# Kernel optimization log

Hardware: AMD Instinct MI355X
Metric: run time of the kernel (lower is better)

The kernel has to match this reference:

```python
import jax, jax.numpy as jnp
import numpy as np

NUM_HEADS = 8
HEAD_DIM = 64
D_MODEL = NUM_HEADS * HEAD_DIM  # 512
B, T = 4, 2048


def setup_inputs() -> dict:
    key = jax.random.key(0)
    k1, k2 = jax.random.split(key)
    x = jax.random.normal(k1, (B, T, D_MODEL), dtype=jnp.float32)
    mask = jnp.ones((B, 1, T, T), dtype=jnp.float32)
    W = jax.random.normal(k2, (D_MODEL, 3 * D_MODEL), dtype=jnp.float32) * (D_MODEL ** -0.5)
    b = jnp.zeros((3 * D_MODEL,), dtype=jnp.float32)
    return {"x": x, "mask": mask, "W": W, "b": b}


def reference(x, mask, W, b):
    batch = x.shape[0]
    # fused QKV projection: [B, T, 3D]
    qkv = jnp.einsum("btd,de->bte", x, W) + b
    # NOTE: faithful to torch reshape [B, T, H, Hd, 3] -> the size-3 axis is innermost
    qkv = qkv.reshape(batch, -1, NUM_HEADS, HEAD_DIM, 3)
    qkv = jnp.transpose(qkv, (4, 0, 2, 1, 3))  # [3, B, H, T, Hd]
    q, k, v = qkv[0], qkv[1], qkv[2]
    logits = jnp.einsum("bhqd,bhkd->bhqk", q, k) / (HEAD_DIM ** 0.5)
    logits = logits + (1.0 - mask) * -10000.0
    w = jax.nn.softmax(logits, axis=-1)
    out = jnp.einsum("bhqk,bhkd->bhqd", w, v)  # [B, H, T, Hd]
    out = jnp.transpose(out, (0, 2, 1, 3)).reshape(batch, -1, NUM_HEADS * HEAD_DIM)
    return out
```

## Files before the change

kernel.cpp:

```cpp
#include <hip/hip_runtime.h>
#include <hip/hip_bf16.h>
#include <stdint.h>

#define B_   4
#define T_   2048
#define H_   8
#define HD_  64
#define DM_  512
#define N3_  1536

typedef short bf_el;
typedef __attribute__((ext_vector_type(8))) bf_el bfrag;
typedef __attribute__((ext_vector_type(4))) float ffrag;

#define SCALE_L2E  0.18033688011112043f
#define MASK_L2E   14426.950408889634f

static __device__ __forceinline__ unsigned short f2bf(float f) {
    union { float f; unsigned int i; } v; v.f = f;
    unsigned int r = v.i + 0x7fff + ((v.i >> 16) & 1);
    return (unsigned short)(r >> 16);
}
static __device__ __forceinline__ unsigned short f2bf_fast(float f) {
    union { float f; unsigned int i; } v; v.f = f;
    return (unsigned short)((v.i + 0x8000u) >> 16);
}

__global__ __launch_bounds__(256) void k_prep(const float* __restrict__ W,
                                              const float* __restrict__ X,
                                              const float* __restrict__ mask,
                                              unsigned short* __restrict__ Wt,
                                              unsigned short* __restrict__ Xb,
                                              int* __restrict__ flags) {
    __shared__ __align__(16) unsigned short Ls[64 * 72];
    const int bid = blockIdx.x;
    const int tid = threadIdx.x;

    if (bid < 512) {
        const int wave = tid >> 6, lane = tid & 63;
        const int e  = bid >> 2;
        const int g  = bid & 3;
        const int mb = e >> 5, qt = e & 31;
#pragma unroll
        for (int w2 = 0; w2 < 2; ++w2) {
            const int kt = g * 8 + wave * 2 + w2;
            unsigned int acc = 0u;
#pragma unroll
            for (int j = 0; j < 16; ++j) {
                const int row = j * 4 + (lane >> 4);
                const uint4 u = *(const uint4*)(mask + ((size_t)mb * T_ + qt * 64 + row) * T_
                                                     + kt * 64 + (lane & 15) * 4);
                acc |= (u.x ^ 0x3F800000u) | (u.y ^ 0x3F800000u) |
                       (u.z ^ 0x3F800000u) | (u.w ^ 0x3F800000u);
            }
            unsigned long long bal = __ballot(acc != 0u);
            if (lane == 0) flags[e * 32 + kt] = (bal != 0ULL) ? 1 : 0;
        }
        return;
    }
    if (bid < 768) {
        const int b2 = bid - 512;
        const float* src = X + (size_t)b2 * 16384;
        unsigned short* dst = Xb + (size_t)b2 * 16384;
#pragma unroll
        for (int j = 0; j < 8; ++j) {
            int idx = j * 512 + tid * 2;
            float4 f0 = *(const float4*)(src + idx * 4);
            float4 f1 = *(const float4*)(src + idx * 4 + 4);
            __align__(16) unsigned short t8[8];
            t8[0] = f2bf_fast(f0.x); t8[1] = f2bf_fast(f0.y);
            t8[2] = f2bf_fast(f0.z); t8[3] = f2bf_fast(f0.w);
            t8[4] = f2bf_fast(f1.x); t8[5] = f2bf_fast(f1.y);
            t8[6] = f2bf_fast(f1.z); t8[7] = f2bf_fast(f1.w);
            *(uint4*)(dst + idx * 4) = *(const uint4*)t8;
        }
        return;
    }
    {
        const int t  = bid - 768;
        const int n0 = (t % 24) * 64;
        const int k0 = (t / 24) * 64;
#pragma unroll
        for (int i = 0; i < 4; ++i) {
            int chunk = tid + i * 256;
            int k = chunk >> 4;
            int c = chunk & 15;
            float4 f = *(const float4*)(W + (size_t)(k0 + k) * N3_ + n0 + c * 4);
            unsigned short* p = Ls + k * 72 + c * 4;
            p[0] = f2bf(f.x); p[1] = f2bf(f.y); p[2] = f2bf(f.z); p[3] = f2bf(f.w);
        }
        __syncthreads();
        const int n = tid >> 2;
        const int g = tid & 3;
        __align__(16) unsigned short tmp[16];
#pragma unroll
        for (int i = 0; i < 16; ++i) tmp[i] = Ls[(g * 16 + i) * 72 + n];
        uint4* dst = (uint4*)(Wt + (size_t)(n0 + n) * DM_ + k0 + g * 16);
        dst[0] = *(const uint4*)(tmp);
        dst[1] = *(const uint4*)(tmp + 8);
    }
}

__global__ __launch_bounds__(256) void k_gemm_qkv(const unsigned short* __restrict__ Xb,
                                                  const unsigned short* __restrict__ Wt,
                                                  const float* __restrict__ bias,
                                                  unsigned short* __restrict__ Qb,
                                                  unsigned short* __restrict__ Kb,
                                                  unsigned short* __restrict__ Vtb) {
    __shared__ __align__(16) unsigned short SH[12800];
    unsigned short* As = SH;
    unsigned short* Bs = SH + 5120;
    unsigned short* Cs = SH;

    const int tid  = threadIdx.x;
    const int wave = tid >> 6;
    const int lane = tid & 63;
    const int quad = lane >> 4;
    const int l16  = lane & 15;
    const int wm = wave >> 1, wn = wave & 1;
    const int m0 = blockIdx.y * 128;
    const int h  = blockIdx.x;
    const int n0 = h * 192;

    float bvv[6];
#pragma unroll
    for (int ni = 0; ni < 6; ++ni) bvv[ni] = bias[n0 + wn * 96 + ni * 16 + l16];

    ffrag acc[4][6];
#pragma unroll
    for (int i = 0; i < 4; ++i)
#pragma unroll
        for (int j = 0; j < 6; ++j) acc[i][j] = (ffrag){0.f, 0.f, 0.f, 0.f};

    for (int kt = 0; kt < 16; ++kt) {
        __syncthreads();
#pragma unroll
        for (int i = 0; i < 2; ++i) {
            int chunk = tid + i * 256;
            int r = chunk >> 2, c = chunk & 3;
            *(uint4*)(As + r * 40 + c * 8) =
                *(const uint4*)(Xb + (size_t)(m0 + r) * DM_ + kt * 32 + c * 8);
        }
#pragma unroll
        for (int i = 0; i < 3; ++i) {
            int chunk = tid + i * 256;
            int r = chunk >> 2, c = chunk & 3;
            *(uint4*)(Bs + r * 40 + c * 8) =
                *(const uint4*)(Wt + (size_t)(n0 + r) * DM_ + kt * 32 + c * 8);
        }
        __syncthreads();
        bfrag af[4], bfr[6];
#pragma unroll
        for (int mi = 0; mi < 4; ++mi)
            af[mi] = *(const bfrag*)(As + (wm * 64 + mi * 16 + l16) * 40 + quad * 8);
#pragma unroll
        for (int ni = 0; ni < 6; ++ni)
            bfr[ni] = *(const bfrag*)(Bs + (wn * 96 + ni * 16 + l16) * 40 + quad * 8);
#pragma unroll
        for (int mi = 0; mi < 4; ++mi)
#pragma unroll
            for (int ni = 0; ni < 6; ++ni)
                acc[mi][ni] = __builtin_amdgcn_mfma_f32_16x16x32_bf16(af[mi], bfr[ni], acc[mi][ni], 0, 0, 0);
    }

    const int b   = m0 >> 11;
    const int tb0 = m0 & 2047;
    const size_t bh = (size_t)(b * 8 + h);
    float cscale[6];
#pragma unroll
    for (int ni = 0; ni < 6; ++ni) {
        int c = wn * 96 + ni * 16 + l16;
        cscale[ni] = (c % 3 == 0) ? SCALE_L2E : 1.0f;
    }
#pragma unroll
    for (int half = 0; half < 2; ++half) {
        __syncthreads();
        if (wm == half) {
#pragma unroll
            for (int mi = 0; mi < 4; ++mi)
#pragma unroll
                for (int ni = 0; ni < 6; ++ni)
#pragma unroll
                    for (int reg = 0; reg < 4; ++reg) {
                        int r = mi * 16 + quad * 4 + reg;
                        int c = wn * 96 + ni * 16 + l16;
                        Cs[r * 200 + c] = f2bf_fast((acc[mi][ni][reg] + bvv[ni]) * cscale[ni]);
                    }
        }
        __syncthreads();
        const int tb = tb0 + half * 64;
#pragma unroll
        for (int i = 0; i < 2; ++i) {
            int idx = tid + i * 256;
            int tl = idx >> 3, hc = (idx & 7) * 8;
            __align__(16) unsigned short tq[8], tk[8];
#pragma unroll
            for (int j = 0; j < 8; ++j) {
                tq[j] = Cs[tl * 200 + (hc + j) * 3 + 0];
                tk[j] = Cs[tl * 200 + (hc + j) * 3 + 1];
            }
            *(uint4*)(Qb + (bh * T_ + tb + tl) * HD_ + hc) = *(const uint4*)tq;
            *(uint4*)(Kb + (bh * T_ + tb + tl) * HD_ + hc) = *(const uint4*)tk;
        }
#pragma unroll
        for (int i = 0; i < 2; ++i) {
            int idx = tid + i * 256;
            int hd = idx >> 3, t8 = (idx & 7) * 8;
            __align__(16) unsigned short tv[8];
#pragma unroll
            for (int j = 0; j < 8; ++j)
                tv[j] = Cs[(t8 + j) * 200 + hd * 3 + 2];
            *(uint4*)(Vtb + (bh * HD_ + hd) * T_ + tb + t8) = *(const uint4*)tv;
        }
    }
}

__global__ __launch_bounds__(256) void k_attn(const unsigned short* __restrict__ Q,
                                              const unsigned short* __restrict__ K,
                                              const unsigned short* __restrict__ Vt,
                                              const float* __restrict__ mask,
                                              const int* __restrict__ flags,
                                              float* __restrict__ out) {
    __shared__ __align__(16) unsigned short Ks[64 * 72];
    __shared__ __align__(16) unsigned short Vs[64 * 72];
    __shared__ __align__(16) unsigned short Ps[4][16 * 72];

    const int tid = threadIdx.x;
    const int wave = tid >> 6, lane = tid & 63;
    const int quad = lane >> 4, l16 = lane & 15;
    const int bh = blockIdx.y, b = bh >> 3, h = bh & 7;
    const int qt = blockIdx.x;
    const int q0 = qt * 128;

    bfrag qf[2][2];
#pragma unroll
    for (int g = 0; g < 2; ++g) {
        size_t qrow = ((size_t)bh * T_ + q0 + wave * 32 + g * 16 + l16) * HD_;
        qf[g][0] = *(const bfrag*)(Q + qrow + quad * 8);
        qf[g][1] = *(const bfrag*)(Q + qrow + 32 + quad * 8);
    }
    float lsum[2][4] = {{0.f,0.f,0.f,0.f},{0.f,0.f,0.f,0.f}};
    ffrag of[2][4];
#pragma unroll
    for (int g = 0; g < 2; ++g)
#pragma unroll
        for (int nb = 0; nb < 4; ++nb) of[g][nb] = (ffrag){0.f, 0.f, 0.f, 0.f};

    const int fbase0 = (b * 32 + qt * 2) * 32;
    const int fbase1 = (b * 32 + qt * 2 + 1) * 32;

    for (int kt = 0; kt < 32; ++kt) {
        __syncthreads();
#pragma unroll
        for (int i = 0; i < 2; ++i) {
            int chunk = tid + i * 256;
            int r = chunk >> 3, c = chunk & 7;
            *(uint4*)(Ks + r * 72 + c * 8) =
                *(const uint4*)(K + ((size_t)bh * T_ + kt * 64 + r) * HD_ + c * 8);
            *(uint4*)(Vs + r * 72 + c * 8) =
                *(const uint4*)(Vt + ((size_t)bh * HD_ + r) * T_ + kt * 64 + c * 8);
        }
        int fl[2];
        fl[0] = flags[fbase0 + kt];
        fl[1] = flags[fbase1 + kt];
        __syncthreads();
        bfrag vf[2][4];
#pragma unroll
        for (int ks = 0; ks < 2; ++ks)
#pragma unroll
            for (int nb = 0; nb < 4; ++nb)
                vf[ks][nb] = *(const bfrag*)(Vs + (nb * 16 + l16) * 72 + (ks * 4 + quad) * 8);

#pragma unroll
        for (int g = 0; g < 2; ++g) {
            ffrag sf[4];
#pragma unroll
            for (int ns = 0; ns < 4; ++ns) {
                ffrag a = (ffrag){0.f, 0.f, 0.f, 0.f};
#pragma unroll
                for (int ks = 0; ks < 2; ++ks) {
                    bfrag kf = *(const bfrag*)(Ks + (ns * 16 + l16) * 72 + (ks * 4 + quad) * 8);
                    a = __builtin_amdgcn_mfma_f32_16x16x32_bf16(qf[g][ks], kf, a, 0, 0, 0);
                }
                sf[ns] = a;
            }
            if (fl[g]) {
#pragma unroll
                for (int reg = 0; reg < 4; ++reg) {
                    int tq = q0 + wave * 32 + g * 16 + quad * 4 + reg;
                    const float* mrow = mask + ((size_t)b * T_ + tq) * T_ + kt * 64;
#pragma unroll
                    for (int ns = 0; ns < 4; ++ns) {
                        float msk = mrow[ns * 16 + l16];
                        float p = __builtin_amdgcn_exp2f(
                            fmaf(msk, MASK_L2E, sf[ns][reg] - MASK_L2E));
                        lsum[g][reg] += p;
                        Ps[wave][(quad * 4 + reg) * 72 + ns * 16 + l16] = f2bf_fast(p);
                    }
                }
            } else {
#pragma unroll
                for (int reg = 0; reg < 4; ++reg) {
#pragma unroll
                    for (int ns = 0; ns < 4; ++ns) {
                        float p = __builtin_amdgcn_exp2f(sf[ns][reg]);
                        lsum[g][reg] += p;
                        Ps[wave][(quad * 4 + reg) * 72 + ns * 16 + l16] = f2bf_fast(p);
                    }
                }
            }
#pragma unroll
            for (int ks = 0; ks < 2; ++ks) {
                bfrag pf = *(const bfrag*)(&Ps[wave][l16 * 72 + (ks * 4 + quad) * 8]);
#pragma unroll
                for (int nb = 0; nb < 4; ++nb)
                    of[g][nb] = __builtin_amdgcn_mfma_f32_16x16x32_bf16(pf, vf[ks][nb], of[g][nb], 0, 0, 0);
            }
        }
    }
#pragma unroll
    for (int g = 0; g < 2; ++g)
#pragma unroll
    for (int reg = 0; reg < 4; ++reg) {
        float s = lsum[g][reg];
#pragma unroll
        for (int d = 1; d < 16; d <<= 1) s += __shfl_xor(s, d, 64);
        float inv = 1.0f / s;
        int t = q0 + wave * 32 + g * 16 + quad * 4 + reg;
#pragma unroll
        for (int nb = 0; nb < 4; ++nb)
            out[((size_t)b * T_ + t) * DM_ + h * 64 + nb * 16 + l16] = of[g][nb][reg] * inv;
    }
}

extern "C" void kernel_launch(void* const* d_in, const int* in_sizes, int n_in,
                              void* d_out, int out_size, void* d_ws, size_t ws_size,
                              hipStream_t stream) {
    const float* X    = (const float*)d_in[0];
    const float* mask = (const float*)d_in[1];
    const float* W    = (const float*)d_in[2];
    const float* bias = (const float*)d_in[3];
    float* outp = (float*)d_out;

    char* ws = (char*)d_ws;
    unsigned short* Wt  = (unsigned short*)(ws);
    unsigned short* Xb  = (unsigned short*)(ws + 1572864);
    unsigned short* Qb  = (unsigned short*)(ws + 9961472);
    unsigned short* Kb  = (unsigned short*)(ws + 18350080);
    unsigned short* Vtb = (unsigned short*)(ws + 26738688);
    int*            flg = (int*)(ws + 35127296);

    k_prep     <<<dim3(960),    256, 0, stream>>>(W, X, mask, Wt, Xb, flg);
    k_gemm_qkv <<<dim3(8, 64),  256, 0, stream>>>(Xb, Wt, bias, Qb, Kb, Vtb);
    k_attn     <<<dim3(16, 32), 256, 0, stream>>>(Qb, Kb, Vtb, mask, flg, outp);
}
```

Measured before the change: 219.6 us.

## Double-buffer K/V tiles in attention, stream mask rows, and reorder block indexing

The attention kernel now keeps two K/V shared-memory buffers. It prefetches the next tile into registers during compute and writes it to the other buffer afterwards, so each iteration needs one barrier instead of two. The mask-scan pass reads full contiguous rows (16 rows per block) and sets tile flags with atomicOr after a memset, replacing strided 64x64 tile reads. The GEMM and attention grids are flattened to 1D with a head-major or bh-minor ordering, meant to improve L2 reuse of shared weights and K/V. The cost is an extra memset launch, some atomics, and more registers and LDS for the prefetch buffers.

```diff
diff --git a/kernel.cpp b/kernel.cpp
--- a/kernel.cpp
+++ b/kernel.cpp
@@ -37,24 +37,28 @@
     const int tid = threadIdx.x;
 
     if (bid < 512) {
+        const int R0 = bid * 16;
+        const int mb = R0 >> 11;
+        const int q0 = R0 & 2047;
+        const int e  = mb * 32 + (q0 >> 6);
         const int wave = tid >> 6, lane = tid & 63;
-        const int e  = bid >> 2;
-        const int g  = bid & 3;
-        const int mb = e >> 5, qt = e & 31;
-#pragma unroll
-        for (int w2 = 0; w2 < 2; ++w2) {
-            const int kt = g * 8 + wave * 2 + w2;
-            unsigned int acc = 0u;
-#pragma unroll
-            for (int j = 0; j < 16; ++j) {
-                const int row = j * 4 + (lane >> 4);
-                const uint4 u = *(const uint4*)(mask + ((size_t)mb * T_ + qt * 64 + row) * T_
-                                                     + kt * 64 + (lane & 15) * 4);
-                acc |= (u.x ^ 0x3F800000u) | (u.y ^ 0x3F800000u) |
-                       (u.z ^ 0x3F800000u) | (u.w ^ 0x3F800000u);
-            }
-            unsigned long long bal = __ballot(acc != 0u);
-            if (lane == 0) flags[e * 32 + kt] = (bal != 0ULL) ? 1 : 0;
+        unsigned int acc = 0u;
+        const float* base = mask + (size_t)R0 * T_ + tid * 8;
+#pragma unroll
+        for (int rr = 0; rr < 16; ++rr) {
+            const uint4 u0 = *(const uint4*)(base + (size_t)rr * T_);
+            const uint4 u1 = *(const uint4*)(base + (size_t)rr * T_ + 4);
+            acc |= (u0.x ^ 0x3F800000u) | (u0.y ^ 0x3F800000u) |
+                   (u0.z ^ 0x3F800000u) | (u0.w ^ 0x3F800000u) |
+                   (u1.x ^ 0x3F800000u) | (u1.y ^ 0x3F800000u) |
+                   (u1.z ^ 0x3F800000u) | (u1.w ^ 0x3F800000u);
+        }
+        unsigned long long bal = __ballot(acc != 0u);
+        if (lane == 0 && bal != 0ULL) {
+#pragma unroll
+            for (int j = 0; j < 8; ++j)
+                if ((bal >> (8 * j)) & 0xFFULL)
+                    atomicOr(&flags[e * 32 + wave * 8 + j], 1);
         }
         return;
     }
@@ -118,8 +122,8 @@
     const int quad = lane >> 4;
     const int l16  = lane & 15;
     const int wm = wave >> 1, wn = wave & 1;
-    const int m0 = blockIdx.y * 128;
-    const int h  = blockIdx.x;
+    const int h  = blockIdx.x >> 6;
+    const int m0 = (blockIdx.x & 63) * 128;
     const int n0 = h * 192;
 
     float bvv[6];
@@ -221,15 +225,15 @@
                                               const float* __restrict__ mask,
                                               const int* __restrict__ flags,
                                               float* __restrict__ out) {
-    __shared__ __align__(16) unsigned short Ks[64 * 72];
-    __shared__ __align__(16) unsigned short Vs[64 * 72];
+    __shared__ __align__(16) unsigned short Ks[2][64 * 72];
+    __shared__ __align__(16) unsigned short Vs[2][64 * 72];
     __shared__ __align__(16) unsigned short Ps[4][16 * 72];
 
     const int tid = threadIdx.x;
     const int wave = tid >> 6, lane = tid & 63;
     const int quad = lane >> 4, l16 = lane & 15;
-    const int bh = blockIdx.y, b = bh >> 3, h = bh & 7;
-    const int qt = blockIdx.x;
+    const int bh = blockIdx.x & 31, b = bh >> 3, h = bh & 7;
+    const int qt = blockIdx.x >> 5;
     const int q0 = qt * 128;
 
     bfrag qf[2][2];
@@ -249,27 +253,40 @@
     const int fbase0 = (b * 32 + qt * 2) * 32;
     const int fbase1 = (b * 32 + qt * 2 + 1) * 32;
 
+    const int sr0 = tid >> 3, sr1 = (tid + 256) >> 3, sc = tid & 7;
+    const unsigned short* Kbase = K  + (size_t)bh * T_ * HD_;
+    const unsigned short* Vbase = Vt + (size_t)bh * HD_ * T_;
+
+    uint4 kreg[2], vreg[2];
+    kreg[0] = *(const uint4*)(Kbase + (size_t)sr0 * HD_ + sc * 8);
+    kreg[1] = *(const uint4*)(Kbase + (size_t)sr1 * HD_ + sc * 8);
+    vreg[0] = *(const uint4*)(Vbase + (size_t)sr0 * T_ + sc * 8);
+    vreg[1] = *(const uint4*)(Vbase + (size_t)sr1 * T_ + sc * 8);
+    *(uint4*)(&Ks[0][sr0 * 72 + sc * 8]) = kreg[0];
+    *(uint4*)(&Ks[0][sr1 * 72 + sc * 8]) = kreg[1];
+    *(uint4*)(&Vs[0][sr0 * 72 + sc * 8]) = vreg[0];
+    *(uint4*)(&Vs[0][sr1 * 72 + sc * 8]) = vreg[1];
+    __syncthreads();
+
     for (int kt = 0; kt < 32; ++kt) {
-        __syncthreads();
-#pragma unroll
-        for (int i = 0; i < 2; ++i) {
-            int chunk = tid + i * 256;
-            int r = chunk >> 3, c = chunk & 7;
-            *(uint4*)(Ks + r * 72 + c * 8) =
-                *(const uint4*)(K + ((size_t)bh * T_ + kt * 64 + r) * HD_ + c * 8);
-            *(uint4*)(Vs + r * 72 + c * 8) =
-                *(const uint4*)(Vt + ((size_t)bh * HD_ + r) * T_ + kt * 64 + c * 8);
+        const int cur = kt & 1;
+        if (kt < 31) {
+            const int kn = (kt + 1) * 64;
+            kreg[0] = *(const uint4*)(Kbase + (size_t)(kn + sr0) * HD_ + sc * 8);
+            kreg[1] = *(const uint4*)(Kbase + (size_t)(kn + sr1) * HD_ + sc * 8);
+            vreg[0] = *(const uint4*)(Vbase + (size_t)sr0 * T_ + kn + sc * 8);
+            vreg[1] = *(const uint4*)(Vbase + (size_t)sr1 * T_ + kn + sc * 8);
         }
         int fl[2];
         fl[0] = flags[fbase0 + kt];
         fl[1] = flags[fbase1 + kt];
-        __syncthreads();
+
         bfrag vf[2][4];
 #pragma unroll
         for (int ks = 0; ks < 2; ++ks)
 #pragma unroll
             for (int nb = 0; nb < 4; ++nb)
-                vf[ks][nb] = *(const bfrag*)(Vs + (nb * 16 + l16) * 72 + (ks * 4 + quad) * 8);
+                vf[ks][nb] = *(const bfrag*)(&Vs[cur][(nb * 16 + l16) * 72 + (ks * 4 + quad) * 8]);
 
 #pragma unroll
         for (int g = 0; g < 2; ++g) {
@@ -279,7 +296,7 @@
                 ffrag a = (ffrag){0.f, 0.f, 0.f, 0.f};
 #pragma unroll
                 for (int ks = 0; ks < 2; ++ks) {
-                    bfrag kf = *(const bfrag*)(Ks + (ns * 16 + l16) * 72 + (ks * 4 + quad) * 8);
+                    bfrag kf = *(const bfrag*)(&Ks[cur][(ns * 16 + l16) * 72 + (ks * 4 + quad) * 8]);
                     a = __builtin_amdgcn_mfma_f32_16x16x32_bf16(qf[g][ks], kf, a, 0, 0, 0);
                 }
                 sf[ns] = a;
@@ -317,6 +334,14 @@
                     of[g][nb] = __builtin_amdgcn_mfma_f32_16x16x32_bf16(pf, vf[ks][nb], of[g][nb], 0, 0, 0);
             }
         }
+        if (kt < 31) {
+            const int nxt = cur ^ 1;
+            *(uint4*)(&Ks[nxt][sr0 * 72 + sc * 8]) = kreg[0];
+            *(uint4*)(&Ks[nxt][sr1 * 72 + sc * 8]) = kreg[1];
+            *(uint4*)(&Vs[nxt][sr0 * 72 + sc * 8]) = vreg[0];
+            *(uint4*)(&Vs[nxt][sr1 * 72 + sc * 8]) = vreg[1];
+            __syncthreads();
+        }
     }
 #pragma unroll
     for (int g = 0; g < 2; ++g)
@@ -350,7 +375,8 @@
     unsigned short* Vtb = (unsigned short*)(ws + 26738688);
     int*            flg = (int*)(ws + 35127296);
 
-    k_prep     <<<dim3(960),    256, 0, stream>>>(W, X, mask, Wt, Xb, flg);
-    k_gemm_qkv <<<dim3(8, 64),  256, 0, stream>>>(Xb, Wt, bias, Qb, Kb, Vtb);
-    k_attn     <<<dim3(16, 32), 256, 0, stream>>>(Qb, Kb, Vtb, mask, flg, outp);
-}
+    hipMemsetAsync(flg, 0, 16384, stream);
+    k_prep     <<<dim3(960), 256, 0, stream>>>(W, X, mask, Wt, Xb, flg);
+    k_gemm_qkv <<<dim3(512), 256, 0, stream>>>(Xb, Wt, bias, Qb, Kb, Vtb);
+    k_attn     <<<dim3(512), 256, 0, stream>>>(Qb, Kb, Vtb, mask, flg, outp);
+}
```

New measurement: 215.8 us. No clear change (-1.7%).
